# Performance work log

Hardware: AMD Instinct MI355X
Metric: run time of the kernel (lower is better)

Reference implementation:

```python
import jax, jax.numpy as jnp
import numpy as np

B = 4          # batch (number of point clouds)
NPER = 50000   # voxels per cloud
G = 96         # voxel grid extent per axis
C = 128        # in_channels
R = 2          # reduction_ratio
K = 27         # 3^3 kernel offsets
BN_EPS = 1e-5


def _build_sparse_geometry(seed=0):
    """Unique voxel coords per sample + 27-neighbor kernel map (Minkowski-style)."""
    rng = np.random.default_rng(seed)
    keys_list = []
    for b in range(B):
        loc = rng.choice(G ** 3, NPER, replace=False)
        loc.sort()
        keys_list.append(b * (G ** 3) + loc)
    keys = np.concatenate(keys_list)  # globally sorted (batch-major)
    N = keys.shape[0]
    loc = keys % (G ** 3)
    xs, ys, zs = loc // (G * G), (loc // G) % G, loc % G
    offsets = [(dx, dy, dz) for dx in (-1, 0, 1) for dy in (-1, 0, 1) for dz in (-1, 0, 1)]
    nbr_idx = np.zeros((N, K), np.int32)
    nbr_mask = np.zeros((N, K), bool)
    for k, (dx, dy, dz) in enumerate(offsets):
        inb = ((xs + dx >= 0) & (xs + dx < G) & (ys + dy >= 0) & (ys + dy < G)
               & (zs + dz >= 0) & (zs + dz < G))
        nkey = keys + dx * G * G + dy * G + dz
        pos = np.searchsorted(keys, nkey)
        pos_c = np.clip(pos, 0, N - 1)
        found = inb & (keys[pos_c] == nkey)
        nbr_idx[:, k] = np.where(found, pos_c, 0)
        nbr_mask[:, k] = found
    batch_idx = np.repeat(np.arange(B), NPER).astype(np.int32)
    return nbr_idx, nbr_mask, batch_idx


def setup_inputs() -> dict:
    nbr_idx, nbr_mask, batch_idx = _build_sparse_geometry(0)
    N = B * NPER
    key = jax.random.key(0)
    ks = jax.random.split(key, 8)
    feats = jax.random.normal(ks[0], (N, C), jnp.float32)
    # channel-attention MLP (MinkowskiLinear has bias=True)
    w1 = jax.random.normal(ks[1], (C, C // R), jnp.float32) * (1.0 / np.sqrt(C))
    b1 = jnp.zeros((C // R,), jnp.float32)
    w2 = jax.random.normal(ks[2], (C // R, C), jnp.float32) * (1.0 / np.sqrt(C // R))
    b2 = jnp.zeros((C,), jnp.float32)
    # spatial attention: 3x3x3 sparse conv C->4 (bias=False), BN(4), 1x1x1 conv 4->4
    conv1_w = jax.random.normal(ks[3], (K, C, 4), jnp.float32) * (1.0 / np.sqrt(K * C))
    bn_gamma = jnp.ones((4,), jnp.float32)
    bn_beta = jnp.zeros((4,), jnp.float32)
    conv2_w = jax.random.normal(ks[4], (4, 4), jnp.float32) * 0.5
    return dict(feats=feats, w1=w1, b1=b1, w2=w2, b2=b2, conv1_w=conv1_w,
                bn_gamma=bn_gamma, bn_beta=bn_beta, conv2_w=conv2_w,
                nbr_idx=jnp.asarray(nbr_idx), nbr_mask=jnp.asarray(nbr_mask),
                batch_idx=jnp.asarray(batch_idx), num_batches=B)


def reference(feats, w1, b1, w2, b2, conv1_w, bn_gamma, bn_beta, conv2_w,
              nbr_idx, nbr_mask, batch_idx, num_batches):
    N = feats.shape[0]
    ones = jnp.ones((N,), feats.dtype)
    counts = jax.ops.segment_sum(ones, batch_idx, num_segments=num_batches,
                                 indices_are_sorted=True)  # [B]
    avg_x = jax.ops.segment_sum(feats, batch_idx, num_segments=num_batches,
                                indices_are_sorted=True) / counts[:, None]  # [B,C]
    max_x = jax.ops.segment_max(feats, batch_idx, num_segments=num_batches,
                                indices_are_sorted=True)  # [B,C]
    mlp = lambda z: jax.nn.relu(z @ w1 + b1) @ w2 + b2
    weights = jax.nn.sigmoid(mlp(avg_x) + mlp(max_x))  # [B,C] channel attention
    # sam_mid: per-sample broadcast multiply
    mid = feats * weights[batch_idx]  # [N,C]
    # sparse 3x3x3 conv C->4 via kernel map (gather + thin matmul per offset)
    mask_f = nbr_mask.astype(feats.dtype)
    y = jnp.zeros((N, 4), feats.dtype)
    for k in range(K):
        y = y + (mid[nbr_idx[:, k]] * mask_f[:, k:k + 1]) @ conv1_w[k]
    # BatchNorm (training-mode batch stats, biased var) + ReLU
    mu = jnp.mean(y, axis=0)
    var = jnp.var(y, axis=0)
    y = (y - mu) * jax.lax.rsqrt(var + BN_EPS) * bn_gamma + bn_beta
    y = jax.nn.relu(y)
    # 1x1x1 conv == linear (bias=False), then sigmoid
    final = jax.nn.sigmoid(y @ conv2_w)  # [N,4]
    # sam_output: max over channels -> scalar spatial gate per point
    gate = jnp.max(final, axis=1, keepdims=True)  # [N,1]
    out = mid * gate + mid + feats
    return out
```

## Files before the change

kernel.cpp:

```cpp
#include <hip/hip_runtime.h>

#define C 128
#define K 27
#define BATCHES 4
#define RA_BPB 512
#define CONV_BLOCKS 512
#define CONV_TPB 1024
#define NWAVES_CONV (CONV_BLOCKS * (CONV_TPB / 64))
#define BN_EPS 1e-5f

typedef __attribute__((ext_vector_type(2))) __fp16 h2;
typedef __attribute__((ext_vector_type(8))) __fp16 h8;

__global__ void detect_mask_kernel(const unsigned int* __restrict__ w, int nwords,
                                   int* __restrict__ flag) {
  int stride = gridDim.x * blockDim.x;
  bool bad = false;
  for (int i = blockIdx.x * blockDim.x + threadIdx.x; i < nwords; i += stride)
    bad |= (w[i] > 1u);
  if (__any(bad) && (threadIdx.x & 63) == 0) atomicOr(flag, 1);
}

__global__ __launch_bounds__(256) void reduceA_kernel(
    const float* __restrict__ feats, float* __restrict__ psum,
    float* __restrict__ pmax, int NPER) {
  int b = blockIdx.x / RA_BPB, chunk = blockIdx.x % RA_BPB;
  int CH = (NPER + RA_BPB - 1) / RA_BPB;
  int r0 = b * NPER + chunk * CH;
  int r1 = min(b * NPER + NPER, r0 + CH);
  int g = threadIdx.x >> 5;
  int l = threadIdx.x & 31;
  float4 s = make_float4(0.f, 0.f, 0.f, 0.f);
  float4 m = make_float4(-INFINITY, -INFINITY, -INFINITY, -INFINITY);
  for (int i = r0 + g; i < r1; i += 8) {
    float4 v = *(const float4*)(feats + (size_t)i * C + l * 4);
    s.x += v.x; s.y += v.y; s.z += v.z; s.w += v.w;
    m.x = fmaxf(m.x, v.x); m.y = fmaxf(m.y, v.y);
    m.z = fmaxf(m.z, v.z); m.w = fmaxf(m.w, v.w);
  }
  __shared__ float ssum[8][C], smax[8][C];
  *(float4*)&ssum[g][l * 4] = s;
  *(float4*)&smax[g][l * 4] = m;
  __syncthreads();
  if (threadIdx.x < C) {
    int c = threadIdx.x;
    float S = 0.f, M = -INFINITY;
#pragma unroll
    for (int gg = 0; gg < 8; ++gg) {
      S += ssum[gg][c];
      M = fmaxf(M, smax[gg][c]);
    }
    psum[(size_t)blockIdx.x * C + c] = S;
    pmax[(size_t)blockIdx.x * C + c] = M;
  }
}

__global__ __launch_bounds__(256) void reduceB_kernel(
    const float* __restrict__ psum, const float* __restrict__ pmax,
    float* __restrict__ avg, float* __restrict__ mx, int NPER) {
  int b = blockIdx.x;
  int g = threadIdx.x >> 5, l = threadIdx.x & 31;
  float4 s = make_float4(0.f, 0.f, 0.f, 0.f);
  float4 m = make_float4(-INFINITY, -INFINITY, -INFINITY, -INFINITY);
  for (int j = g; j < RA_BPB; j += 8) {
    size_t base = (size_t)(b * RA_BPB + j) * C + l * 4;
    float4 vs = *(const float4*)(psum + base);
    float4 vm = *(const float4*)(pmax + base);
    s.x += vs.x; s.y += vs.y; s.z += vs.z; s.w += vs.w;
    m.x = fmaxf(m.x, vm.x); m.y = fmaxf(m.y, vm.y);
    m.z = fmaxf(m.z, vm.z); m.w = fmaxf(m.w, vm.w);
  }
  __shared__ float ssum[8][C], smax[8][C];
  *(float4*)&ssum[g][l * 4] = s;
  *(float4*)&smax[g][l * 4] = m;
  __syncthreads();
  if (threadIdx.x < C) {
    int c = threadIdx.x;
    float S = 0.f, M = -INFINITY;
#pragma unroll
    for (int gg = 0; gg < 8; ++gg) {
      S += ssum[gg][c];
      M = fmaxf(M, smax[gg][c]);
    }
    avg[b * C + c] = S / (float)NPER;
    mx[b * C + c] = M;
  }
}

__global__ void mlp_kernel(const float* __restrict__ avg, const float* __restrict__ mx,
                           const float* __restrict__ w1, const float* __restrict__ b1,
                           const float* __restrict__ w2, const float* __restrict__ b2,
                           float* __restrict__ wgt) {
  int b = blockIdx.x, t = threadIdx.x;
  __shared__ float h1a[64], h1m[64];
  if (t < 64) {
    float sa = b1[t], sm = b1[t];
    for (int c = 0; c < C; ++c) {
      float wv = w1[c * 64 + t];
      sa += avg[b * C + c] * wv;
      sm += mx[b * C + c] * wv;
    }
    h1a[t] = fmaxf(sa, 0.f);
    h1m[t] = fmaxf(sm, 0.f);
  }
  __syncthreads();
  float za = b2[t], zm = b2[t];
  for (int h = 0; h < 64; ++h) {
    float wv = w2[h * C + t];
    za += h1a[h] * wv;
    zm += h1m[h] * wv;
  }
  float z = za + zm;
  wgt[b * C + t] = 1.f / (1.f + expf(-z));
}

__global__ __launch_bounds__(CONV_TPB, 8) void conv_kernel(
    const float* __restrict__ feats, const float* __restrict__ wgt,
    const float* __restrict__ conv1_w, const int* __restrict__ nbr_idx,
    const void* __restrict__ nbr_mask, const int* __restrict__ flagp,
    float* __restrict__ y, float* __restrict__ bnpart, int N, int NPER) {
  __shared__ __align__(16) h8 wlds[K * 64];
  int tid = threadIdx.x;
  for (int e = tid; e < K * 64; e += CONV_TPB) {
    float4 A = ((const float4*)conv1_w)[e * 2];
    float4 B = ((const float4*)conv1_w)[e * 2 + 1];
    h8 w;
    h2 p;
    p = __builtin_amdgcn_cvt_pkrtz(A.x, B.x); w[0] = p[0]; w[1] = p[1];
    p = __builtin_amdgcn_cvt_pkrtz(A.y, B.y); w[2] = p[0]; w[3] = p[1];
    p = __builtin_amdgcn_cvt_pkrtz(A.z, B.z); w[4] = p[0]; w[5] = p[1];
    p = __builtin_amdgcn_cvt_pkrtz(A.w, B.w); w[6] = p[0]; w[7] = p[1];
    wlds[e] = w;
  }
  __syncthreads();

  int lane = tid & 63;
  int g = lane >> 4, cl = lane & 15;
  int gwave = blockIdx.x * (CONV_TPB / 64) + (tid >> 6);
  int nwaves = gridDim.x * (CONV_TPB / 64);
  int rpw = (N + nwaves - 1) / nwaves;
  int rbeg = gwave * rpw, rend = min(N, rbeg + rpw);
  bool byteMode = (*flagp != 0);
  const unsigned char* mb = (const unsigned char*)nbr_mask;
  const int* mi = (const int*)nbr_mask;

  int bB = min(rbeg / NPER, BATCHES - 1);
  int bEnd = (bB + 1) * NPER;
  float2 wr = *(const float2*)(wgt + bB * C + 2 * lane);

  bool mk = false;
  int jl = 0;
  if (rbeg < rend && lane < K) {
    size_t e = (size_t)rbeg * K + lane;
    mk = byteMode ? (mb[e] != 0) : (mi[e] != 0);
    jl = nbr_idx[e];
  }

  float sAcc = 0.f, qAcc = 0.f;

  unsigned balTailN = 0, balTailP = 0;
  int jN = 0, jP = 0, cntN = 0, cntP = 0;
  int k0N = 0, k1N = 0, k2N = 0, k3N = 0, k0P = 0, k1P = 0, k2P = 0, k3P = 0;
  float2 g0N = make_float2(0, 0), g1N = g0N, g2N = g0N, g3N = g0N;
  float2 g0P = g0N, g1P = g0N, g2P = g0N, g3P = g0N;

#define FRONT(iF)                                                           \
  do {                                                                      \
    unsigned bb = (unsigned)__ballot(mk);                                   \
    jN = jl;                                                                \
    mk = false;                                                             \
    if ((iF) + 1 < rend && lane < K) {                                      \
      size_t e = (size_t)((iF) + 1) * K + lane;                             \
      mk = byteMode ? (mb[e] != 0) : (mi[e] != 0);                          \
      jl = nbr_idx[e];                                                      \
    }                                                                       \
    cntN = __popc(bb);                                                      \
    k0N = __ffs(bb) - 1; bb &= bb - 1;                                      \
    k1N = __ffs(bb) - 1; bb &= bb - 1;                                      \
    k2N = __ffs(bb) - 1; bb &= bb - 1;                                      \
    k3N = __ffs(bb) - 1; bb &= bb - 1;                                      \
    balTailN = bb;                                                          \
    int j0 = __shfl(jN, k0N & 63);                                          \
    int j1 = __shfl(jN, k1N & 63);                                          \
    int j2 = __shfl(jN, k2N & 63);                                          \
    int j3 = __shfl(jN, k3N & 63);                                          \
    if (cntN > 0) g0N = *(const float2*)(feats + (size_t)j0 * C + 2 * lane);\
    if (cntN > 1) g1N = *(const float2*)(feats + (size_t)j1 * C + 2 * lane);\
    if (cntN > 2) g2N = *(const float2*)(feats + (size_t)j2 * C + 2 * lane);\
    if (cntN > 3) g3N = *(const float2*)(feats + (size_t)j3 * C + 2 * lane);\
  } while (0)

#define ACCD(ff, kk)                                                        \
  {                                                                         \
    h2 fp = __builtin_amdgcn_cvt_pkrtz(ff.x * wr.x, ff.y * wr.y);           \
    h8 w = wlds[(kk)*64 + lane];                                            \
    h2 w0 = __builtin_shufflevector(w, w, 0, 1);                            \
    h2 w1 = __builtin_shufflevector(w, w, 2, 3);                            \
    h2 w2 = __builtin_shufflevector(w, w, 4, 5);                            \
    h2 w3 = __builtin_shufflevector(w, w, 6, 7);                            \
    a0 = __builtin_amdgcn_fdot2(fp, w0, a0, false);                         \
    a1 = __builtin_amdgcn_fdot2(fp, w1, a1, false);                         \
    a2 = __builtin_amdgcn_fdot2(fp, w2, a2, false);                         \
    a3 = __builtin_amdgcn_fdot2(fp, w3, a3, false);                         \
  }

#define BACK(ir)                                                            \
  do {                                                                      \
    if ((ir) >= bEnd && bB < BATCHES - 1) {                                 \
      ++bB; bEnd += NPER;                                                   \
      wr = *(const float2*)(wgt + bB * C + 2 * lane);                       \
    }                                                                       \
    float a0 = 0, a1 = 0, a2 = 0, a3 = 0;                                   \
    if (cntP > 0) ACCD(g0P, k0P)                                            \
    if (cntP > 1) ACCD(g1P, k1P)                                            \
    if (cntP > 2) ACCD(g2P, k2P)                                            \
    if (cntP > 3) ACCD(g3P, k3P)                                            \
    unsigned bt = balTailP;                                                 \
    while (bt) {                                                            \
      int kk = __ffs(bt) - 1; bt &= bt - 1;                                 \
      int jj = __shfl(jP, kk);                                              \
      float2 f = *(const float2*)(feats + (size_t)jj * C + 2 * lane);       \
      ACCD(f, kk)                                                           \
    }                                                                       \
    a0 += __shfl_xor(a0, 16); a1 += __shfl_xor(a1, 16);                     \
    a2 += __shfl_xor(a2, 16); a3 += __shfl_xor(a3, 16);                     \
    a0 += __shfl_xor(a0, 32); a1 += __shfl_xor(a1, 32);                     \
    a2 += __shfl_xor(a2, 32); a3 += __shfl_xor(a3, 32);                     \
    float v = (g == 0) ? a0 : (g == 1) ? a1 : (g == 2) ? a2 : a3;           \
    v += __shfl_xor(v, 1);                                                  \
    v += __shfl_xor(v, 2);                                                  \
    v += __shfl_xor(v, 4);                                                  \
    v += __shfl_xor(v, 8);                                                  \
    if (cl == 0) y[(size_t)(ir)*4 + g] = v;                                 \
    sAcc += v; qAcc += v * v;                                               \
  } while (0)

#define ROTATE()                                                            \
  do {                                                                      \
    balTailP = balTailN; jP = jN; cntP = cntN;                              \
    k0P = k0N; k1P = k1N; k2P = k2N; k3P = k3N;                             \
    g0P = g0N; g1P = g1N; g2P = g2N; g3P = g3N;                             \
  } while (0)

  if (rbeg < rend) {
    FRONT(rbeg);
    ROTATE();
    for (int i = rbeg + 1; i < rend; ++i) {
      FRONT(i);
      BACK(i - 1);
      ROTATE();
    }
    BACK(rend - 1);
  }
#undef FRONT
#undef ACCD
#undef BACK
#undef ROTATE

  if (cl == 0) {
    float* p = bnpart + (size_t)gwave * 8;
    p[g] = sAcc;
    p[4 + g] = qAcc;
  }
}

__global__ void bn_reduce_kernel(const float* __restrict__ bnpart, int nparts,
                                 const float* __restrict__ gamma, const float* __restrict__ beta,
                                 float* __restrict__ scsh, int N) {
  __shared__ float red[256 * 8];
  int t = threadIdx.x;
  float S[8];
#pragma unroll
  for (int o = 0; o < 8; ++o) S[o] = 0.f;
  for (int i = t; i < nparts; i += 256) {
#pragma unroll
    for (int o = 0; o < 8; ++o) S[o] += bnpart[(size_t)i * 8 + o];
  }
#pragma unroll
  for (int o = 0; o < 8; ++o) red[t * 8 + o] = S[o];
  __syncthreads();
  for (int st = 128; st > 0; st >>= 1) {
    if (t < st) {
#pragma unroll
      for (int o = 0; o < 8; ++o) red[t * 8 + o] += red[(t + st) * 8 + o];
    }
    __syncthreads();
  }
  if (t == 0) {
    float invN = 1.f / (float)N;
#pragma unroll
    for (int o = 0; o < 4; ++o) {
      float mu = red[o] * invN;
      float var = red[4 + o] * invN - mu * mu;
      float sc = gamma[o] * rsqrtf(var + BN_EPS);
      scsh[o] = sc;
      scsh[4 + o] = beta[o] - mu * sc;
    }
  }
}

__global__ void final_kernel(const float* __restrict__ feats, const float* __restrict__ wgt,
                             const float* __restrict__ y, const float* __restrict__ scsh,
                             const float* __restrict__ c2, float* __restrict__ out,
                             int N, int NPER) {
  int lane = threadIdx.x & 63;
  int gwave = blockIdx.x * (blockDim.x >> 6) + (threadIdx.x >> 6);
  int nwaves = gridDim.x * (blockDim.x >> 6);
  int rpw = (N + nwaves - 1) / nwaves;
  int rbeg = gwave * rpw, rend = min(N, rbeg + rpw);
  float4 sc = *(const float4*)scsh;
  float4 sh = *(const float4*)(scsh + 4);
  float4 r0 = *(const float4*)(c2 + 0);
  float4 r1 = *(const float4*)(c2 + 4);
  float4 r2 = *(const float4*)(c2 + 8);
  float4 r3 = *(const float4*)(c2 + 12);
  for (int i = rbeg; i < rend; ++i) {
    float4 yv = *(const float4*)(y + (size_t)i * 4);
    float y0 = fmaxf(yv.x * sc.x + sh.x, 0.f);
    float y1 = fmaxf(yv.y * sc.y + sh.y, 0.f);
    float y2 = fmaxf(yv.z * sc.z + sh.z, 0.f);
    float y3 = fmaxf(yv.w * sc.w + sh.w, 0.f);
    float z0 = y0 * r0.x + y1 * r1.x + y2 * r2.x + y3 * r3.x;
    float z1 = y0 * r0.y + y1 * r1.y + y2 * r2.y + y3 * r3.y;
    float z2 = y0 * r0.z + y1 * r1.z + y2 * r2.z + y3 * r3.z;
    float z3 = y0 * r0.w + y1 * r1.w + y2 * r2.w + y3 * r3.w;
    float zm = fmaxf(fmaxf(z0, z1), fmaxf(z2, z3));
    float gate = 1.f / (1.f + expf(-zm));
    float g1 = 1.f + gate;
    int b = i / NPER;
    float2 w = *(const float2*)(wgt + b * C + 2 * lane);
    float2 f = *(const float2*)(feats + (size_t)i * C + 2 * lane);
    float2 o2;
    o2.x = f.x * (1.f + w.x * g1);
    o2.y = f.y * (1.f + w.y * g1);
    *(float2*)(out + (size_t)i * C + 2 * lane) = o2;
  }
}

extern "C" void kernel_launch(void* const* d_in, const int* in_sizes, int n_in,
                              void* d_out, int out_size, void* d_ws, size_t ws_size,
                              hipStream_t stream) {
  const float* feats   = (const float*)d_in[0];
  const float* w1      = (const float*)d_in[1];
  const float* b1      = (const float*)d_in[2];
  const float* w2      = (const float*)d_in[3];
  const float* b2      = (const float*)d_in[4];
  const float* conv1w  = (const float*)d_in[5];
  const float* gamma   = (const float*)d_in[6];
  const float* beta    = (const float*)d_in[7];
  const float* c2      = (const float*)d_in[8];
  const int*   nbr_idx = (const int*)d_in[9];
  const void*  nbr_mask = d_in[10];
  int N = in_sizes[0] / C;
  int NPER = N / BATCHES;

  char* ws = (char*)d_ws;
  size_t off = 0;
  int* flag = (int*)(ws + off);        off += 16;
  float* psum = (float*)(ws + off);    off += (size_t)BATCHES * RA_BPB * C * 4;
  float* pmax = (float*)(ws + off);    off += (size_t)BATCHES * RA_BPB * C * 4;
  float* avg  = (float*)(ws + off);    off += (size_t)BATCHES * C * 4;
  float* mx   = (float*)(ws + off);    off += (size_t)BATCHES * C * 4;
  float* wgt  = (float*)(ws + off);    off += (size_t)BATCHES * C * 4;
  float* y    = (float*)(ws + off);    off += (size_t)N * 4 * 4;
  float* bnpart = (float*)(ws + off);  off += (size_t)NWAVES_CONV * 8 * 4;
  float* scsh = (float*)(ws + off);    off += 64;
  float* outp = (float*)d_out;

  int nwords = (N * K) / 4;
  if (nwords > (1 << 20)) nwords = 1 << 20;
  hipMemsetAsync(flag, 0, sizeof(int), stream);
  detect_mask_kernel<<<64, 256, 0, stream>>>((const unsigned int*)nbr_mask, nwords, flag);
  reduceA_kernel<<<BATCHES * RA_BPB, 256, 0, stream>>>(feats, psum, pmax, NPER);
  reduceB_kernel<<<BATCHES, 256, 0, stream>>>(psum, pmax, avg, mx, NPER);
  mlp_kernel<<<BATCHES, C, 0, stream>>>(avg, mx, w1, b1, w2, b2, wgt);
  conv_kernel<<<CONV_BLOCKS, CONV_TPB, 0, stream>>>(feats, wgt, conv1w, nbr_idx, nbr_mask,
                                                    flag, y, bnpart, N, NPER);
  bn_reduce_kernel<<<1, 256, 0, stream>>>(bnpart, NWAVES_CONV, gamma, beta, scsh, N);
  final_kernel<<<2048, 256, 0, stream>>>(feats, wgt, y, scsh, c2, outp, N, NPER);
}
```

Before: 178.9 us.

## Deepen conv gather pipeline to three rows and fuse mask detection into reduction

The sparse conv loop now keeps three rows in flight: mask/index loads run three rows ahead and the feature gathers for a row are issued before the previous rows are accumulated. This is meant to hide gather latency better, at the cost of more registers per thread. The separate mask-format detection kernel is folded into reduceA, removing one launch; the reduction loop is unrolled by two and the final kernel prefetches the next row and tracks the batch weight incrementally. The fused mask check reads a fixed 2048x512 words, which may differ from the old capped range.

```diff
diff --git a/kernel.cpp b/kernel.cpp
--- a/kernel.cpp
+++ b/kernel.cpp
@@ -12,18 +12,16 @@
 typedef __attribute__((ext_vector_type(2))) __fp16 h2;
 typedef __attribute__((ext_vector_type(8))) __fp16 h8;
 
-__global__ void detect_mask_kernel(const unsigned int* __restrict__ w, int nwords,
-                                   int* __restrict__ flag) {
-  int stride = gridDim.x * blockDim.x;
-  bool bad = false;
-  for (int i = blockIdx.x * blockDim.x + threadIdx.x; i < nwords; i += stride)
-    bad |= (w[i] > 1u);
-  if (__any(bad) && (threadIdx.x & 63) == 0) atomicOr(flag, 1);
-}
-
 __global__ __launch_bounds__(256) void reduceA_kernel(
     const float* __restrict__ feats, float* __restrict__ psum,
-    float* __restrict__ pmax, int NPER) {
+    float* __restrict__ pmax, const unsigned int* __restrict__ mwords,
+    int* __restrict__ flag, int NPER) {
+  int base = blockIdx.x * 512;
+  bool bad = false;
+  bad |= (mwords[base + threadIdx.x] > 1u);
+  bad |= (mwords[base + 256 + threadIdx.x] > 1u);
+  if (__any(bad) && (threadIdx.x & 63) == 0) atomicOr(flag, 1);
+
   int b = blockIdx.x / RA_BPB, chunk = blockIdx.x % RA_BPB;
   int CH = (NPER + RA_BPB - 1) / RA_BPB;
   int r0 = b * NPER + chunk * CH;
@@ -32,7 +30,16 @@
   int l = threadIdx.x & 31;
   float4 s = make_float4(0.f, 0.f, 0.f, 0.f);
   float4 m = make_float4(-INFINITY, -INFINITY, -INFINITY, -INFINITY);
-  for (int i = r0 + g; i < r1; i += 8) {
+  int i = r0 + g;
+  for (; i + 8 < r1; i += 16) {
+    float4 v1 = *(const float4*)(feats + (size_t)i * C + l * 4);
+    float4 v2 = *(const float4*)(feats + (size_t)(i + 8) * C + l * 4);
+    s.x += v1.x + v2.x; s.y += v1.y + v2.y;
+    s.z += v1.z + v2.z; s.w += v1.w + v2.w;
+    m.x = fmaxf(m.x, fmaxf(v1.x, v2.x)); m.y = fmaxf(m.y, fmaxf(v1.y, v2.y));
+    m.z = fmaxf(m.z, fmaxf(v1.z, v2.z)); m.w = fmaxf(m.w, fmaxf(v1.w, v2.w));
+  }
+  if (i < r1) {
     float4 v = *(const float4*)(feats + (size_t)i * C + l * 4);
     s.x += v.x; s.y += v.y; s.z += v.z; s.w += v.w;
     m.x = fmaxf(m.x, v.x); m.y = fmaxf(m.y, v.y);
@@ -148,46 +155,48 @@
   int bEnd = (bB + 1) * NPER;
   float2 wr = *(const float2*)(wgt + bB * C + 2 * lane);
 
-  bool mk = false;
-  int jl = 0;
-  if (rbeg < rend && lane < K) {
-    size_t e = (size_t)rbeg * K + lane;
-    mk = byteMode ? (mb[e] != 0) : (mi[e] != 0);
-    jl = nbr_idx[e];
-  }
-
   float sAcc = 0.f, qAcc = 0.f;
 
-  unsigned balTailN = 0, balTailP = 0;
-  int jN = 0, jP = 0, cntN = 0, cntP = 0;
-  int k0N = 0, k1N = 0, k2N = 0, k3N = 0, k0P = 0, k1P = 0, k2P = 0, k3P = 0;
-  float2 g0N = make_float2(0, 0), g1N = g0N, g2N = g0N, g3N = g0N;
-  float2 g0P = g0N, g1P = g0N, g2P = g0N, g3P = g0N;
-
-#define FRONT(iF)                                                           \
+  bool mk0 = false, mk1 = false, mk2 = false;
+  int jl0 = 0, jl1 = 0, jl2 = 0;
+  unsigned tail0 = 0, tail1 = 0, tail2 = 0;
+  int jj0 = 0, jj1 = 0, jj2 = 0, cnt0 = 0, cnt1 = 0, cnt2 = 0;
+  int k00 = 0, k10 = 0, k20 = 0, k30 = 0;
+  int k01 = 0, k11 = 0, k21 = 0, k31 = 0;
+  int k02 = 0, k12 = 0, k22 = 0, k32 = 0;
+  float2 g00, g10, g20, g30, g01, g11, g21, g31, g02, g12, g22, g32;
+  g00 = g10 = g20 = g30 = g01 = g11 = g21 = g31 = g02 = g12 = g22 = g32 =
+      make_float2(0.f, 0.f);
+
+#define MLOAD(S, row)                                                       \
   do {                                                                      \
-    unsigned bb = (unsigned)__ballot(mk);                                   \
-    jN = jl;                                                                \
-    mk = false;                                                             \
-    if ((iF) + 1 < rend && lane < K) {                                      \
-      size_t e = (size_t)((iF) + 1) * K + lane;                             \
-      mk = byteMode ? (mb[e] != 0) : (mi[e] != 0);                          \
-      jl = nbr_idx[e];                                                      \
+    mk##S = false;                                                          \
+    if ((row) < rend && lane < K) {                                         \
+      size_t e = (size_t)(row)*K + lane;                                    \
+      mk##S = byteMode ? (mb[e] != 0) : (mi[e] != 0);                       \
+      jl##S = nbr_idx[e];                                                   \
     }                                                                       \
-    cntN = __popc(bb);                                                      \
-    k0N = __ffs(bb) - 1; bb &= bb - 1;                                      \
-    k1N = __ffs(bb) - 1; bb &= bb - 1;                                      \
-    k2N = __ffs(bb) - 1; bb &= bb - 1;                                      \
-    k3N = __ffs(bb) - 1; bb &= bb - 1;                                      \
-    balTailN = bb;                                                          \
-    int j0 = __shfl(jN, k0N & 63);                                          \
-    int j1 = __shfl(jN, k1N & 63);                                          \
-    int j2 = __shfl(jN, k2N & 63);                                          \
-    int j3 = __shfl(jN, k3N & 63);                                          \
-    if (cntN > 0) g0N = *(const float2*)(feats + (size_t)j0 * C + 2 * lane);\
-    if (cntN > 1) g1N = *(const float2*)(feats + (size_t)j1 * C + 2 * lane);\
-    if (cntN > 2) g2N = *(const float2*)(feats + (size_t)j2 * C + 2 * lane);\
-    if (cntN > 3) g3N = *(const float2*)(feats + (size_t)j3 * C + 2 * lane);\
+  } while (0)
+
+#define FRONT(S, iF)                                                        \
+  do {                                                                      \
+    unsigned bb = (unsigned)__ballot(mk##S);                                \
+    jj##S = jl##S;                                                          \
+    MLOAD(S, (iF) + 3);                                                     \
+    cnt##S = __popc(bb);                                                    \
+    k0##S = __ffs(bb) - 1; bb &= bb - 1;                                    \
+    k1##S = __ffs(bb) - 1; bb &= bb - 1;                                    \
+    k2##S = __ffs(bb) - 1; bb &= bb - 1;                                    \
+    k3##S = __ffs(bb) - 1; bb &= bb - 1;                                    \
+    tail##S = bb;                                                           \
+    int j0 = __shfl(jj##S, k0##S & 63);                                     \
+    int j1 = __shfl(jj##S, k1##S & 63);                                     \
+    int j2 = __shfl(jj##S, k2##S & 63);                                     \
+    int j3 = __shfl(jj##S, k3##S & 63);                                     \
+    if (cnt##S > 0) g0##S = *(const float2*)(feats + (size_t)j0 * C + 2 * lane); \
+    if (cnt##S > 1) g1##S = *(const float2*)(feats + (size_t)j1 * C + 2 * lane); \
+    if (cnt##S > 2) g2##S = *(const float2*)(feats + (size_t)j2 * C + 2 * lane); \
+    if (cnt##S > 3) g3##S = *(const float2*)(feats + (size_t)j3 * C + 2 * lane); \
   } while (0)
 
 #define ACCD(ff, kk)                                                        \
@@ -204,58 +213,59 @@
     a3 = __builtin_amdgcn_fdot2(fp, w3, a3, false);                         \
   }
 
-#define BACK(ir)                                                            \
+#define BACK(S, ir)                                                         \
   do {                                                                      \
-    if ((ir) >= bEnd && bB < BATCHES - 1) {                                 \
-      ++bB; bEnd += NPER;                                                   \
-      wr = *(const float2*)(wgt + bB * C + 2 * lane);                       \
+    if ((ir) < rend) {                                                      \
+      if ((ir) >= bEnd && bB < BATCHES - 1) {                               \
+        ++bB; bEnd += NPER;                                                 \
+        wr = *(const float2*)(wgt + bB * C + 2 * lane);                     \
+      }                                                                     \
+      float a0 = 0, a1 = 0, a2 = 0, a3 = 0;                                 \
+      if (cnt##S > 0) ACCD(g0##S, k0##S)                                    \
+      if (cnt##S > 1) ACCD(g1##S, k1##S)                                    \
+      if (cnt##S > 2) ACCD(g2##S, k2##S)                                    \
+      if (cnt##S > 3) ACCD(g3##S, k3##S)                                    \
+      unsigned bt = tail##S;                                                \
+      while (bt) {                                                          \
+        int kk = __ffs(bt) - 1; bt &= bt - 1;                               \
+        int jj = __shfl(jj##S, kk);                                         \
+        float2 f = *(const float2*)(feats + (size_t)jj * C + 2 * lane);     \
+        ACCD(f, kk)                                                         \
+      }                                                                     \
+      a0 += __shfl_xor(a0, 16); a1 += __shfl_xor(a1, 16);                   \
+      a2 += __shfl_xor(a2, 16); a3 += __shfl_xor(a3, 16);                   \
+      a0 += __shfl_xor(a0, 32); a1 += __shfl_xor(a1, 32);                   \
+      a2 += __shfl_xor(a2, 32); a3 += __shfl_xor(a3, 32);                   \
+      float v = (g == 0) ? a0 : (g == 1) ? a1 : (g == 2) ? a2 : a3;         \
+      v += __shfl_xor(v, 1);                                                \
+      v += __shfl_xor(v, 2);                                                \
+      v += __shfl_xor(v, 4);                                                \
+      v += __shfl_xor(v, 8);                                                \
+      if (cl == 0) y[(size_t)(ir)*4 + g] = v;                               \
+      sAcc += v; qAcc += v * v;                                             \
     }                                                                       \
-    float a0 = 0, a1 = 0, a2 = 0, a3 = 0;                                   \
-    if (cntP > 0) ACCD(g0P, k0P)                                            \
-    if (cntP > 1) ACCD(g1P, k1P)                                            \
-    if (cntP > 2) ACCD(g2P, k2P)                                            \
-    if (cntP > 3) ACCD(g3P, k3P)                                            \
-    unsigned bt = balTailP;                                                 \
-    while (bt) {                                                            \
-      int kk = __ffs(bt) - 1; bt &= bt - 1;                                 \
-      int jj = __shfl(jP, kk);                                              \
-      float2 f = *(const float2*)(feats + (size_t)jj * C + 2 * lane);       \
-      ACCD(f, kk)                                                           \
-    }                                                                       \
-    a0 += __shfl_xor(a0, 16); a1 += __shfl_xor(a1, 16);                     \
-    a2 += __shfl_xor(a2, 16); a3 += __shfl_xor(a3, 16);                     \
-    a0 += __shfl_xor(a0, 32); a1 += __shfl_xor(a1, 32);                     \
-    a2 += __shfl_xor(a2, 32); a3 += __shfl_xor(a3, 32);                     \
-    float v = (g == 0) ? a0 : (g == 1) ? a1 : (g == 2) ? a2 : a3;           \
-    v += __shfl_xor(v, 1);                                                  \
-    v += __shfl_xor(v, 2);                                                  \
-    v += __shfl_xor(v, 4);                                                  \
-    v += __shfl_xor(v, 8);                                                  \
-    if (cl == 0) y[(size_t)(ir)*4 + g] = v;                                 \
-    sAcc += v; qAcc += v * v;                                               \
   } while (0)
 
-#define ROTATE()                                                            \
-  do {                                                                      \
-    balTailP = balTailN; jP = jN; cntP = cntN;                              \
-    k0P = k0N; k1P = k1N; k2P = k2N; k3P = k3N;                             \
-    g0P = g0N; g1P = g1N; g2P = g2N; g3P = g3N;                             \
-  } while (0)
-
   if (rbeg < rend) {
-    FRONT(rbeg);
-    ROTATE();
-    for (int i = rbeg + 1; i < rend; ++i) {
-      FRONT(i);
-      BACK(i - 1);
-      ROTATE();
-    }
-    BACK(rend - 1);
-  }
+    MLOAD(0, rbeg);
+    MLOAD(1, rbeg + 1);
+    MLOAD(2, rbeg + 2);
+    FRONT(0, rbeg);
+    FRONT(1, rbeg + 1);
+    FRONT(2, rbeg + 2);
+    for (int i = rbeg; i < rend; i += 3) {
+      BACK(0, i);
+      FRONT(0, i + 3);
+      BACK(1, i + 1);
+      FRONT(1, i + 4);
+      BACK(2, i + 2);
+      FRONT(2, i + 5);
+    }
+  }
+#undef MLOAD
 #undef FRONT
 #undef ACCD
 #undef BACK
-#undef ROTATE
 
   if (cl == 0) {
     float* p = bnpart + (size_t)gwave * 8;
@@ -299,23 +309,39 @@
   }
 }
 
-__global__ void final_kernel(const float* __restrict__ feats, const float* __restrict__ wgt,
-                             const float* __restrict__ y, const float* __restrict__ scsh,
-                             const float* __restrict__ c2, float* __restrict__ out,
-                             int N, int NPER) {
+__global__ __launch_bounds__(256) void final_kernel(
+    const float* __restrict__ feats, const float* __restrict__ wgt,
+    const float* __restrict__ y, const float* __restrict__ scsh,
+    const float* __restrict__ c2, float* __restrict__ out, int N, int NPER) {
   int lane = threadIdx.x & 63;
   int gwave = blockIdx.x * (blockDim.x >> 6) + (threadIdx.x >> 6);
   int nwaves = gridDim.x * (blockDim.x >> 6);
   int rpw = (N + nwaves - 1) / nwaves;
   int rbeg = gwave * rpw, rend = min(N, rbeg + rpw);
+  if (rbeg >= rend) return;
   float4 sc = *(const float4*)scsh;
   float4 sh = *(const float4*)(scsh + 4);
   float4 r0 = *(const float4*)(c2 + 0);
   float4 r1 = *(const float4*)(c2 + 4);
   float4 r2 = *(const float4*)(c2 + 8);
   float4 r3 = *(const float4*)(c2 + 12);
+  int bB = min(rbeg / NPER, BATCHES - 1);
+  int bEnd = (bB + 1) * NPER;
+  float2 w = *(const float2*)(wgt + bB * C + 2 * lane);
+
+  float4 yvN = *(const float4*)(y + (size_t)rbeg * 4);
+  float2 fN = *(const float2*)(feats + (size_t)rbeg * C + 2 * lane);
   for (int i = rbeg; i < rend; ++i) {
-    float4 yv = *(const float4*)(y + (size_t)i * 4);
+    float4 yv = yvN;
+    float2 f = fN;
+    if (i + 1 < rend) {
+      yvN = *(const float4*)(y + (size_t)(i + 1) * 4);
+      fN = *(const float2*)(feats + (size_t)(i + 1) * C + 2 * lane);
+    }
+    if (i >= bEnd && bB < BATCHES - 1) {
+      ++bB; bEnd += NPER;
+      w = *(const float2*)(wgt + bB * C + 2 * lane);
+    }
     float y0 = fmaxf(yv.x * sc.x + sh.x, 0.f);
     float y1 = fmaxf(yv.y * sc.y + sh.y, 0.f);
     float y2 = fmaxf(yv.z * sc.z + sh.z, 0.f);
@@ -327,9 +353,6 @@
     float zm = fmaxf(fmaxf(z0, z1), fmaxf(z2, z3));
     float gate = 1.f / (1.f + expf(-zm));
     float g1 = 1.f + gate;
-    int b = i / NPER;
-    float2 w = *(const float2*)(wgt + b * C + 2 * lane);
-    float2 f = *(const float2*)(feats + (size_t)i * C + 2 * lane);
     float2 o2;
     o2.x = f.x * (1.f + w.x * g1);
     o2.y = f.y * (1.f + w.y * g1);
@@ -367,11 +390,9 @@
   float* scsh = (float*)(ws + off);    off += 64;
   float* outp = (float*)d_out;
 
-  int nwords = (N * K) / 4;
-  if (nwords > (1 << 20)) nwords = 1 << 20;
   hipMemsetAsync(flag, 0, sizeof(int), stream);
-  detect_mask_kernel<<<64, 256, 0, stream>>>((const unsigned int*)nbr_mask, nwords, flag);
-  reduceA_kernel<<<BATCHES * RA_BPB, 256, 0, stream>>>(feats, psum, pmax, NPER);
+  reduceA_kernel<<<BATCHES * RA_BPB, 256, 0, stream>>>(
+      feats, psum, pmax, (const unsigned int*)nbr_mask, flag, NPER);
   reduceB_kernel<<<BATCHES, 256, 0, stream>>>(psum, pmax, avg, mx, NPER);
   mlp_kernel<<<BATCHES, C, 0, stream>>>(avg, mx, w1, b1, w2, b2, wgt);
   conv_kernel<<<CONV_BLOCKS, CONV_TPB, 0, stream>>>(feats, wgt, conv1w, nbr_idx, nbr_mask,
```

Result: slower. 212.4 us (+18.8%).
